# Kernel optimization log

Measured on AMD Instinct MI355X. Metric: run time of the kernel, lower is better.

The kernel has to match this reference:

```python
import jax, jax.numpy as jnp
import numpy as np

HEAD_SIZE = 64

def setup_inputs() -> dict:
    key = jax.random.key(0)
    k1, k2, k3, k4 = jax.random.split(key, 4)
    B, T, C = 4, 4096, 1024
    x = jax.random.normal(k1, (B, T, C), dtype=jnp.float32)
    Wk = jax.random.normal(k2, (C, HEAD_SIZE), dtype=jnp.float32) * (C ** -0.5)
    Wq = jax.random.normal(k3, (C, HEAD_SIZE), dtype=jnp.float32) * (C ** -0.5)
    Wv = jax.random.normal(k4, (C, HEAD_SIZE), dtype=jnp.float32) * (C ** -0.5)
    return {"x": x, "Wk": Wk, "Wq": Wq, "Wv": Wv}

def reference(x, Wk, Wq, Wv):
    # x: [B, T, C]; projections to [B, T, H]
    T = x.shape[1]
    k = jnp.einsum('btc,ch->bth', x, Wk)
    q = jnp.einsum('btc,ch->bth', x, Wq)
    v = jnp.einsum('btc,ch->bth', x, Wv)
    scale = jnp.asarray(HEAD_SIZE ** -0.5, dtype=x.dtype)
    scores = jnp.einsum('bqh,bkh->bqk', q, k) * scale  # [B, T, T]
    causal = jnp.tril(jnp.ones((T, T), dtype=bool))
    scores = jnp.where(causal, scores, jnp.asarray(-jnp.inf, dtype=scores.dtype))
    attn = jax.nn.softmax(scores, axis=-1)  # dropout is identity in eval mode
    out = jnp.einsum('bqk,bkh->bqh', attn, v)
    return out
```

## Files before the change

### kernel.cpp

```cpp
#include <hip/hip_runtime.h>
#include <hip/hip_bf16.h>
#include <math.h>

#define NB 4
#define NT 4096
#define NC 1024
#define NH 64

typedef __attribute__((ext_vector_type(8))) short short8;
typedef __attribute__((ext_vector_type(4))) float f32x4;
typedef __attribute__((ext_vector_type(8))) unsigned short ushort8v;
typedef __attribute__((ext_vector_type(4))) unsigned short ushort4v;

static __device__ __forceinline__ unsigned short f2bf(float f) {
    union { __hip_bfloat16 b; unsigned short u; } cv;
    cv.b = __float2bfloat16(f);
    return cv.u;
}

__global__ __launch_bounds__(256) void wprep_kernel(
    const float* __restrict__ Wk,
    const float* __restrict__ Wq,
    const float* __restrict__ Wv,
    unsigned short* __restrict__ wt)
{
    __shared__ float tile[64][65];
    const int m  = blockIdx.x >> 4;
    const int k0 = (blockIdx.x & 15) << 6;
    const float* __restrict__ W = (m == 0) ? Wk : (m == 1) ? Wq : Wv;
    const float qs = (m == 1) ? 0.125f * 1.44269504f : 1.0f;
    const int tid = threadIdx.x;
    const int c   = tid & 63;
    for (int i = tid >> 6; i < 64; i += 4)
        tile[i][c] = W[(size_t)(k0 + i) * NH + c];
    __syncthreads();
    const int i0 = (tid >> 6) * 16;
    unsigned short* dst = wt + ((size_t)m * 64 + c) * NC + k0 + i0;
    ushort8v a, b;
#pragma unroll
    for (int j = 0; j < 8; ++j) a[j] = f2bf(tile[i0 + j][c] * qs);
#pragma unroll
    for (int j = 0; j < 8; ++j) b[j] = f2bf(tile[i0 + 8 + j][c] * qs);
    *reinterpret_cast<ushort8v*>(dst)     = a;
    *reinterpret_cast<ushort8v*>(dst + 8) = b;
}

__global__ __launch_bounds__(256, 2) void proj_kernel(
    const float* __restrict__ x,
    const unsigned short* __restrict__ wt,
    unsigned short* __restrict__ ko,
    unsigned short* __restrict__ qo,
    unsigned short* __restrict__ vt)
{
    __shared__ unsigned short xsb[2][32 * 64];
    __shared__ unsigned short wsb[2][192 * 64];

    const int tid  = threadIdx.x;
    const int wid  = tid >> 6;
    const int lane = tid & 63;
    const int l15  = lane & 15;
    const int hi   = lane >> 4;
    const int t0   = blockIdx.x << 5;

    const int srow = tid >> 3;
    const int sg   = tid & 7;
    const int ssw  = sg ^ (srow & 7);
    const float* __restrict__ xsrc = x + (size_t)(t0 + srow) * NC + sg * 8;
    unsigned short* const sdst0 = &xsb[0][srow * 64 + ssw * 8];
    unsigned short* const sdst1 = &xsb[1][srow * 64 + ssw * 8];

    int wrow[6], wsl[6];
#pragma unroll
    for (int it = 0; it < 6; ++it) {
        const int F = it * 256 + tid;
        wrow[it] = F >> 3;
        wsl[it]  = F & 7;
    }

    int mm[3], hr[3];
#pragma unroll
    for (int f = 0; f < 3; ++f) {
        const int hc = wid * 48 + f * 16;
        mm[f] = hc >> 6;
        hr[f] = hc & 63;
    }

    f32x4 acc[2][3];
#pragma unroll
    for (int mf = 0; mf < 2; ++mf)
#pragma unroll
        for (int f = 0; f < 3; ++f) acc[mf][f] = (f32x4){0.f, 0.f, 0.f, 0.f};

    auto XWRITE = [&](unsigned short* dst, const f32x4& a, const f32x4& b) {
        ushort8v pk;
        pk[0] = f2bf(a[0]); pk[1] = f2bf(a[1]);
        pk[2] = f2bf(a[2]); pk[3] = f2bf(a[3]);
        pk[4] = f2bf(b[0]); pk[5] = f2bf(b[1]);
        pk[6] = f2bf(b[2]); pk[7] = f2bf(b[3]);
        *reinterpret_cast<ushort8v*>(dst) = pk;
    };

    auto WSTORE = [&](int bi, const short8 (&wr)[6]) {
#pragma unroll
        for (int it = 0; it < 6; ++it) {
            const int dst = wrow[it] * 64 + ((wsl[it] ^ (wrow[it] & 7)) << 3);
            *reinterpret_cast<short8*>(&wsb[bi][dst]) = wr[it];
        }
    };

    auto COMPUTE = [&](int bi) {
        short8 xf[2][2];
#pragma unroll
        for (int mf = 0; mf < 2; ++mf) {
            const int row = mf * 16 + l15;
#pragma unroll
            for (int ks = 0; ks < 2; ++ks) {
                const int sw = (ks * 4 + hi) ^ (row & 7);
                xf[mf][ks] = *reinterpret_cast<const short8*>(
                    &xsb[bi][row * 64 + sw * 8]);
            }
        }
#pragma unroll
        for (int f = 0; f < 3; ++f) {
            const int wr = wid * 48 + f * 16 + l15;
            const int r7 = l15 & 7;
#pragma unroll
            for (int ks = 0; ks < 2; ++ks) {
                const short8 wf = *reinterpret_cast<const short8*>(
                    &wsb[bi][wr * 64 + (((hi + ks * 4) ^ r7) << 3)]);
                if (mm[f] == 2) {
#pragma unroll
                    for (int mf = 0; mf < 2; ++mf)
                        acc[mf][f] = __builtin_amdgcn_mfma_f32_16x16x32_bf16(
                            xf[mf][ks], wf, acc[mf][f], 0, 0, 0);
                } else {
#pragma unroll
                    for (int mf = 0; mf < 2; ++mf)
                        acc[mf][f] = __builtin_amdgcn_mfma_f32_16x16x32_bf16(
                            wf, xf[mf][ks], acc[mf][f], 0, 0, 0);
                }
            }
        }
    };

    {
        const f32x4 a = *reinterpret_cast<const f32x4*>(xsrc);
        const f32x4 b = *reinterpret_cast<const f32x4*>(xsrc + 4);
        XWRITE(sdst0, a, b);
        short8 wr[6];
#pragma unroll
        for (int it = 0; it < 6; ++it)
            wr[it] = *reinterpret_cast<const short8*>(
                wt + (size_t)wrow[it] * NC + wsl[it] * 8);
        WSTORE(0, wr);
    }
    __syncthreads();

    for (int ck = 0; ck < 16; ++ck) {
        const int cur = ck & 1;
        f32x4 na, nb;
        short8 wr[6];
        if (ck < 15) {
            const float* p = xsrc + (ck + 1) * 64;
            na = *reinterpret_cast<const f32x4*>(p);
            nb = *reinterpret_cast<const f32x4*>(p + 4);
#pragma unroll
            for (int it = 0; it < 6; ++it)
                wr[it] = *reinterpret_cast<const short8*>(
                    wt + (size_t)wrow[it] * NC + (ck + 1) * 64 + wsl[it] * 8);
        }
        COMPUTE(cur);
        if (ck < 15) {
            XWRITE(cur ? sdst0 : sdst1, na, nb);
            WSTORE(cur ^ 1, wr);
        }
        __syncthreads();
    }

    const int b  = t0 >> 12;
    const int tl = t0 & (NT - 1);
#pragma unroll
    for (int f = 0; f < 3; ++f) {
#pragma unroll
        for (int mf = 0; mf < 2; ++mf) {
            const f32x4 a = acc[mf][f];
            ushort4v pk;
            pk[0] = f2bf(a[0]); pk[1] = f2bf(a[1]);
            pk[2] = f2bf(a[2]); pk[3] = f2bf(a[3]);
            if (mm[f] == 2) {
                unsigned short* d = vt + ((size_t)(b * NH + hr[f] + l15)) * NT
                                       + tl + mf * 16 + hi * 4;
                *reinterpret_cast<ushort4v*>(d) = pk;
            } else {
                unsigned short* o = (mm[f] == 0) ? ko : qo;
                unsigned short* d = o + (size_t)(t0 + mf * 16 + l15) * NH
                                      + hr[f] + hi * 4;
                *reinterpret_cast<ushort4v*>(d) = pk;
            }
        }
    }
}

__global__ __launch_bounds__(512) void attn_kernel(
    const unsigned short* __restrict__ kin,
    const unsigned short* __restrict__ qin,
    const unsigned short* __restrict__ vt,
    float* __restrict__ part)
{
    __shared__ unsigned short ksb[2][64 * 64];
    __shared__ unsigned short vsb[2][64 * 64];
    __shared__ unsigned short p_lds[8][16 * 72];

    const int tid  = threadIdx.x;
    const int wid  = tid >> 6;
    const int lane = tid & 63;
    const int q15  = lane & 15;
    const int hi   = lane >> 4;

    const int bid  = blockIdx.x;
    const int xcd  = bid & 7;
    const int b    = xcd >> 1;
    const int clin = ((bid >> 3) << 1) | (xcd & 1);
    const int c    = 143 - clin;

    int qi = 0, basei = 0;
    for (int t = 31; t >= 0; --t) {
        const int g = t >> 2, r = t & 3;
        const int bs = t + 2 * g * (g - 1) + r * g;
        if (bs <= c) { qi = t; basei = bs; break; }
    }
    const int k     = c - basei;
    const int n_blk = 2 * qi + 2;
    const int jb0   = k * 8;
    const int jend  = min(jb0 + 8, n_blk);
    const int n_w   = 2 * qi + 1 + (wid >> 2);

    const unsigned short* kb = kin + (size_t)b * NT * NH;
    const unsigned short* qb = qin + (size_t)b * NT * NH;
    const unsigned short* vb = vt  + (size_t)b * NH * NT;

    const int gq = qi * 128 + wid * 16 + q15;

    short8 qf0, qf1;
    {
        const unsigned short* qrow = qb + (size_t)gq * NH + hi * 8;
        qf0 = *reinterpret_cast<const short8*>(qrow);
        qf1 = *reinterpret_cast<const short8*>(qrow + 32);
    }

    const int srow = tid >> 3;
    const int sg   = tid & 7;
    const int sdst = srow * 64 + (sg ^ (srow & 7)) * 8;
    const unsigned short* kstat = kb + (size_t)srow * NH + sg * 8;
    const unsigned short* vstat = vb + (size_t)srow * NT + sg * 8;

    f32x4 ot[4];
#pragma unroll
    for (int i = 0; i < 4; ++i) ot[i] = (f32x4){0.f, 0.f, 0.f, 0.f};
    float m = 0.f, lp = 0.f;

    {
        const short8 kr = *reinterpret_cast<const short8*>(kstat + (size_t)jb0 * 4096);
        const short8 vr = *reinterpret_cast<const short8*>(vstat + jb0 * 64);
        *reinterpret_cast<short8*>(&ksb[0][sdst]) = kr;
        *reinterpret_cast<short8*>(&vsb[0][sdst]) = vr;
    }
    __syncthreads();

    int cur = 0;
    for (int jb = jb0; jb < jend; ++jb) {
        const bool more = (jb + 1 < jend);
        short8 knx, vnx;
        if (more) {
            knx = *reinterpret_cast<const short8*>(kstat + (size_t)(jb + 1) * 4096);
            vnx = *reinterpret_cast<const short8*>(vstat + (jb + 1) * 64);
        }

        if (jb < n_w) {
            const int kv0 = jb << 6;
            const int r7  = q15 & 7;

            f32x4 st[4];
#pragma unroll
            for (int kt = 0; kt < 4; ++kt) {
                const int rb = (kt * 16 + q15) * 64;
                const short8 ka0 = *reinterpret_cast<const short8*>(
                    &ksb[cur][rb + ((hi ^ r7) * 8)]);
                const short8 ka1 = *reinterpret_cast<const short8*>(
                    &ksb[cur][rb + (((4 + hi) ^ r7) * 8)]);
                f32x4 acc = (f32x4){0.f, 0.f, 0.f, 0.f};
                acc = __builtin_amdgcn_mfma_f32_16x16x32_bf16(ka0, qf0, acc, 0, 0, 0);
                acc = __builtin_amdgcn_mfma_f32_16x16x32_bf16(ka1, qf1, acc, 0, 0, 0);
                st[kt] = acc;
            }

            float tmax4 = -INFINITY;
            if (jb == n_w - 1) {
#pragma unroll
                for (int kt = 0; kt < 4; ++kt)
#pragma unroll
                    for (int r = 0; r < 4; ++r) {
                        const int gk = kv0 + kt * 16 + hi * 4 + r;
                        const float s = (gk <= gq) ? st[kt][r] : -INFINITY;
                        st[kt][r] = s;
                        tmax4 = fmaxf(tmax4, s);
                    }
            } else {
#pragma unroll
                for (int kt = 0; kt < 4; ++kt)
#pragma unroll
                    for (int r = 0; r < 4; ++r)
                        tmax4 = fmaxf(tmax4, st[kt][r]);
            }

            if (!__all(tmax4 <= m + 11.5f)) {
                float tm = fmaxf(tmax4, __shfl_xor(tmax4, 16));
                tm = fmaxf(tm, __shfl_xor(tm, 32));
                const float mnew = fmaxf(m, tm);
                const float corr = __builtin_amdgcn_exp2f(m - mnew);
                lp *= corr;
#pragma unroll
                for (int i = 0; i < 4; ++i) {
                    ot[i][0] *= corr; ot[i][1] *= corr;
                    ot[i][2] *= corr; ot[i][3] *= corr;
                }
                m = mnew;
            }

#pragma unroll
            for (int kt = 0; kt < 4; ++kt) {
                const float p0 = __builtin_amdgcn_exp2f(st[kt][0] - m);
                const float p1 = __builtin_amdgcn_exp2f(st[kt][1] - m);
                const float p2 = __builtin_amdgcn_exp2f(st[kt][2] - m);
                const float p3 = __builtin_amdgcn_exp2f(st[kt][3] - m);
                lp += (p0 + p1) + (p2 + p3);
                ushort4v pk;
                pk[0] = f2bf(p0); pk[1] = f2bf(p1);
                pk[2] = f2bf(p2); pk[3] = f2bf(p3);
                *reinterpret_cast<ushort4v*>(&p_lds[wid][q15 * 72 + kt * 16 + hi * 4]) = pk;
            }

            const short8 pb0 = *reinterpret_cast<const short8*>(&p_lds[wid][q15 * 72 + hi * 8]);
            const short8 pb1 = *reinterpret_cast<const short8*>(&p_lds[wid][q15 * 72 + 32 + hi * 8]);
#pragma unroll
            for (int ht = 0; ht < 4; ++ht) {
                const int rb = (ht * 16 + q15) * 64;
                const short8 va0 = *reinterpret_cast<const short8*>(
                    &vsb[cur][rb + ((hi ^ r7) * 8)]);
                const short8 va1 = *reinterpret_cast<const short8*>(
                    &vsb[cur][rb + (((4 + hi) ^ r7) * 8)]);
                ot[ht] = __builtin_amdgcn_mfma_f32_16x16x32_bf16(va0, pb0, ot[ht], 0, 0, 0);
                ot[ht] = __builtin_amdgcn_mfma_f32_16x16x32_bf16(va1, pb1, ot[ht], 0, 0, 0);
            }
        }

        if (more) {
            *reinterpret_cast<short8*>(&ksb[cur ^ 1][sdst]) = knx;
            *reinterpret_cast<short8*>(&vsb[cur ^ 1][sdst]) = vnx;
        }
        __syncthreads();
        cur ^= 1;
    }

    float l = lp + __shfl_xor(lp, 16);
    l += __shfl_xor(l, 32);
    float* pp = part + (((size_t)b * 144 + c) * 128 + wid * 16 + q15) * 68;
#pragma unroll
    for (int ht = 0; ht < 4; ++ht)
        *reinterpret_cast<f32x4*>(pp + ht * 16 + hi * 4) = ot[ht];
    if (hi == 0) { pp[64] = m; pp[65] = l; }
}

__global__ __launch_bounds__(256) void comb_kernel(
    const float* __restrict__ part,
    float* __restrict__ outp)
{
    const int tid = threadIdx.x;
    const int bid = blockIdx.x;
    const int b   = bid >> 10;
    const int lr  = ((bid & 1023) << 2) + (tid >> 6);
    const int h   = tid & 63;
    const int qi  = lr >> 7;
    const int g   = qi >> 2, r = qi & 3;
    const int basei = qi + 2 * g * (g - 1) + r * g;
    const int nch   = (qi >> 2) + 1;
    const float* p0 = part + (((size_t)b * 144 + basei) * 128 + (lr & 127)) * 68;

    float mg = -INFINITY;
    for (int ch = 0; ch < nch; ++ch)
        mg = fmaxf(mg, p0[(size_t)ch * 128 * 68 + 64]);
    float L = 0.f, o = 0.f;
    for (int ch = 0; ch < nch; ++ch) {
        const float* pc = p0 + (size_t)ch * 128 * 68;
        const float w = __builtin_amdgcn_exp2f(pc[64] - mg);
        L += w * pc[65];
        o += w * pc[h];
    }
    outp[((size_t)b * NT + lr) * NH + h] = o / L;
}

extern "C" void kernel_launch(void* const* d_in, const int* in_sizes, int n_in,
                              void* d_out, int out_size, void* d_ws, size_t ws_size,
                              hipStream_t stream) {
    const float* x  = (const float*)d_in[0];
    const float* Wk = (const float*)d_in[1];
    const float* Wq = (const float*)d_in[2];
    const float* Wv = (const float*)d_in[3];
    float* out = (float*)d_out;

    unsigned short* kbuf = (unsigned short*)d_ws;
    unsigned short* qbuf = kbuf + (size_t)NB * NT * NH;
    unsigned short* vtbf = qbuf + (size_t)NB * NT * NH;
    unsigned short* wtbf = vtbf + (size_t)NB * NT * NH;
    float* part = (float*)(wtbf + (size_t)3 * 64 * NC);

    wprep_kernel<<<48, 256, 0, stream>>>(Wk, Wq, Wv, wtbf);
    proj_kernel<<<NB * NT / 32, 256, 0, stream>>>(x, wtbf, kbuf, qbuf, vtbf);
    attn_kernel<<<576, 512, 0, stream>>>(kbuf, qbuf, vtbf, part);
    comb_kernel<<<4096, 256, 0, stream>>>(part, out);
}
```

Before: 67.10 us.

## Process two query tiles per wave in attention, halving block size

Each wave now handles 32 query rows as two 16-row tiles instead of one, so a block of 4 waves (256 threads) covers the same 128 queries that 8 waves did before. Every K/V fragment read from LDS is reused for two MFMA groups, halving LDS traffic per FLOP, and each thread stages two rows of K/V per tile. The cost is more registers per thread (two accumulators, score sets and softmax states) and fewer waves per block to hide latency.

Measured after the change: 73.02 us. 8.8% more time.

```diff
diff --git a/kernel.cpp b/kernel.cpp
--- a/kernel.cpp
+++ b/kernel.cpp
@@ -6,6 +6,7 @@
 #define NT 4096
 #define NC 1024
 #define NH 64
+#define NCH 144
 
 typedef __attribute__((ext_vector_type(8))) short short8;
 typedef __attribute__((ext_vector_type(4))) float f32x4;
@@ -201,7 +202,7 @@
     }
 }
 
-__global__ __launch_bounds__(512) void attn_kernel(
+__global__ __launch_bounds__(256) void attn_kernel(
     const unsigned short* __restrict__ kin,
     const unsigned short* __restrict__ qin,
     const unsigned short* __restrict__ vt,
@@ -221,7 +222,7 @@
     const int xcd  = bid & 7;
     const int b    = xcd >> 1;
     const int clin = ((bid >> 3) << 1) | (xcd & 1);
-    const int c    = 143 - clin;
+    const int c    = (NCH - 1) - clin;
 
     int qi = 0, basei = 0;
     for (int t = 31; t >= 0; --t) {
@@ -233,54 +234,67 @@
     const int n_blk = 2 * qi + 2;
     const int jb0   = k * 8;
     const int jend  = min(jb0 + 8, n_blk);
-    const int n_w   = 2 * qi + 1 + (wid >> 2);
+    const int n_w   = 2 * qi + 1 + (wid >> 1);
 
     const unsigned short* kb = kin + (size_t)b * NT * NH;
     const unsigned short* qb = qin + (size_t)b * NT * NH;
     const unsigned short* vb = vt  + (size_t)b * NH * NT;
 
-    const int gq = qi * 128 + wid * 16 + q15;
-
-    short8 qf0, qf1;
-    {
-        const unsigned short* qrow = qb + (size_t)gq * NH + hi * 8;
-        qf0 = *reinterpret_cast<const short8*>(qrow);
-        qf1 = *reinterpret_cast<const short8*>(qrow + 32);
+    const int gqb = qi * 128 + wid * 32 + q15;
+
+    short8 qf[2][2];
+#pragma unroll
+    for (int qc = 0; qc < 2; ++qc) {
+        const unsigned short* qrow = qb + (size_t)(gqb + qc * 16) * NH + hi * 8;
+        qf[qc][0] = *reinterpret_cast<const short8*>(qrow);
+        qf[qc][1] = *reinterpret_cast<const short8*>(qrow + 32);
     }
 
     const int srow = tid >> 3;
     const int sg   = tid & 7;
-    const int sdst = srow * 64 + (sg ^ (srow & 7)) * 8;
-    const unsigned short* kstat = kb + (size_t)srow * NH + sg * 8;
-    const unsigned short* vstat = vb + (size_t)srow * NT + sg * 8;
-
-    f32x4 ot[4];
-#pragma unroll
-    for (int i = 0; i < 4; ++i) ot[i] = (f32x4){0.f, 0.f, 0.f, 0.f};
-    float m = 0.f, lp = 0.f;
+    const int ssw  = (sg ^ (srow & 7)) * 8;
+    const int sdA  = srow * 64 + ssw;
+    const int sdB  = (srow + 32) * 64 + ssw;
+    const unsigned short* kstA = kb + (size_t)srow * NH + sg * 8;
+    const unsigned short* kstB = kb + (size_t)(srow + 32) * NH + sg * 8;
+    const unsigned short* vstA = vb + (size_t)srow * NT + sg * 8;
+    const unsigned short* vstB = vb + (size_t)(srow + 32) * NT + sg * 8;
+
+    f32x4 ot[2][4];
+#pragma unroll
+    for (int qc = 0; qc < 2; ++qc)
+#pragma unroll
+        for (int i = 0; i < 4; ++i) ot[qc][i] = (f32x4){0.f, 0.f, 0.f, 0.f};
+    float m0 = 0.f, m1 = 0.f, lp0 = 0.f, lp1 = 0.f;
 
     {
-        const short8 kr = *reinterpret_cast<const short8*>(kstat + (size_t)jb0 * 4096);
-        const short8 vr = *reinterpret_cast<const short8*>(vstat + jb0 * 64);
-        *reinterpret_cast<short8*>(&ksb[0][sdst]) = kr;
-        *reinterpret_cast<short8*>(&vsb[0][sdst]) = vr;
+        *reinterpret_cast<short8*>(&ksb[0][sdA]) =
+            *reinterpret_cast<const short8*>(kstA + (size_t)jb0 * 4096);
+        *reinterpret_cast<short8*>(&ksb[0][sdB]) =
+            *reinterpret_cast<const short8*>(kstB + (size_t)jb0 * 4096);
+        *reinterpret_cast<short8*>(&vsb[0][sdA]) =
+            *reinterpret_cast<const short8*>(vstA + jb0 * 64);
+        *reinterpret_cast<short8*>(&vsb[0][sdB]) =
+            *reinterpret_cast<const short8*>(vstB + jb0 * 64);
     }
     __syncthreads();
 
     int cur = 0;
     for (int jb = jb0; jb < jend; ++jb) {
         const bool more = (jb + 1 < jend);
-        short8 knx, vnx;
+        short8 ka_n, kb_n, va_n, vb_n;
         if (more) {
-            knx = *reinterpret_cast<const short8*>(kstat + (size_t)(jb + 1) * 4096);
-            vnx = *reinterpret_cast<const short8*>(vstat + (jb + 1) * 64);
+            ka_n = *reinterpret_cast<const short8*>(kstA + (size_t)(jb + 1) * 4096);
+            kb_n = *reinterpret_cast<const short8*>(kstB + (size_t)(jb + 1) * 4096);
+            va_n = *reinterpret_cast<const short8*>(vstA + (jb + 1) * 64);
+            vb_n = *reinterpret_cast<const short8*>(vstB + (jb + 1) * 64);
         }
 
         if (jb < n_w) {
             const int kv0 = jb << 6;
             const int r7  = q15 & 7;
 
-            f32x4 st[4];
+            f32x4 st[2][4];
 #pragma unroll
             for (int kt = 0; kt < 4; ++kt) {
                 const int rb = (kt * 16 + q15) * 64;
@@ -288,60 +302,88 @@
                     &ksb[cur][rb + ((hi ^ r7) * 8)]);
                 const short8 ka1 = *reinterpret_cast<const short8*>(
                     &ksb[cur][rb + (((4 + hi) ^ r7) * 8)]);
-                f32x4 acc = (f32x4){0.f, 0.f, 0.f, 0.f};
-                acc = __builtin_amdgcn_mfma_f32_16x16x32_bf16(ka0, qf0, acc, 0, 0, 0);
-                acc = __builtin_amdgcn_mfma_f32_16x16x32_bf16(ka1, qf1, acc, 0, 0, 0);
-                st[kt] = acc;
-            }
-
-            float tmax4 = -INFINITY;
+#pragma unroll
+                for (int qc = 0; qc < 2; ++qc) {
+                    f32x4 acc = (f32x4){0.f, 0.f, 0.f, 0.f};
+                    acc = __builtin_amdgcn_mfma_f32_16x16x32_bf16(ka0, qf[qc][0], acc, 0, 0, 0);
+                    acc = __builtin_amdgcn_mfma_f32_16x16x32_bf16(ka1, qf[qc][1], acc, 0, 0, 0);
+                    st[qc][kt] = acc;
+                }
+            }
+
+            float tx0 = -INFINITY, tx1 = -INFINITY;
             if (jb == n_w - 1) {
 #pragma unroll
                 for (int kt = 0; kt < 4; ++kt)
 #pragma unroll
                     for (int r = 0; r < 4; ++r) {
                         const int gk = kv0 + kt * 16 + hi * 4 + r;
-                        const float s = (gk <= gq) ? st[kt][r] : -INFINITY;
-                        st[kt][r] = s;
-                        tmax4 = fmaxf(tmax4, s);
+                        float s0 = (gk <= gqb)      ? st[0][kt][r] : -INFINITY;
+                        float s1 = (gk <= gqb + 16) ? st[1][kt][r] : -INFINITY;
+                        st[0][kt][r] = s0; st[1][kt][r] = s1;
+                        tx0 = fmaxf(tx0, s0); tx1 = fmaxf(tx1, s1);
                     }
             } else {
 #pragma unroll
                 for (int kt = 0; kt < 4; ++kt)
 #pragma unroll
-                    for (int r = 0; r < 4; ++r)
-                        tmax4 = fmaxf(tmax4, st[kt][r]);
-            }
-
-            if (!__all(tmax4 <= m + 11.5f)) {
-                float tm = fmaxf(tmax4, __shfl_xor(tmax4, 16));
+                    for (int r = 0; r < 4; ++r) {
+                        tx0 = fmaxf(tx0, st[0][kt][r]);
+                        tx1 = fmaxf(tx1, st[1][kt][r]);
+                    }
+            }
+
+            if (!__all(tx0 <= m0 + 11.5f)) {
+                float tm = fmaxf(tx0, __shfl_xor(tx0, 16));
                 tm = fmaxf(tm, __shfl_xor(tm, 32));
-                const float mnew = fmaxf(m, tm);
-                const float corr = __builtin_amdgcn_exp2f(m - mnew);
-                lp *= corr;
+                const float mnew = fmaxf(m0, tm);
+                const float corr = __builtin_amdgcn_exp2f(m0 - mnew);
+                lp0 *= corr;
 #pragma unroll
                 for (int i = 0; i < 4; ++i) {
-                    ot[i][0] *= corr; ot[i][1] *= corr;
-                    ot[i][2] *= corr; ot[i][3] *= corr;
+                    ot[0][i][0] *= corr; ot[0][i][1] *= corr;
+                    ot[0][i][2] *= corr; ot[0][i][3] *= corr;
                 }
-                m = mnew;
-            }
-
-#pragma unroll
-            for (int kt = 0; kt < 4; ++kt) {
-                const float p0 = __builtin_amdgcn_exp2f(st[kt][0] - m);
-                const float p1 = __builtin_amdgcn_exp2f(st[kt][1] - m);
-                const float p2 = __builtin_amdgcn_exp2f(st[kt][2] - m);
-                const float p3 = __builtin_amdgcn_exp2f(st[kt][3] - m);
-                lp += (p0 + p1) + (p2 + p3);
-                ushort4v pk;
-                pk[0] = f2bf(p0); pk[1] = f2bf(p1);
-                pk[2] = f2bf(p2); pk[3] = f2bf(p3);
-                *reinterpret_cast<ushort4v*>(&p_lds[wid][q15 * 72 + kt * 16 + hi * 4]) = pk;
-            }
-
-            const short8 pb0 = *reinterpret_cast<const short8*>(&p_lds[wid][q15 * 72 + hi * 8]);
-            const short8 pb1 = *reinterpret_cast<const short8*>(&p_lds[wid][q15 * 72 + 32 + hi * 8]);
+                m0 = mnew;
+            }
+            if (!__all(tx1 <= m1 + 11.5f)) {
+                float tm = fmaxf(tx1, __shfl_xor(tx1, 16));
+                tm = fmaxf(tm, __shfl_xor(tm, 32));
+                const float mnew = fmaxf(m1, tm);
+                const float corr = __builtin_amdgcn_exp2f(m1 - mnew);
+                lp1 *= corr;
+#pragma unroll
+                for (int i = 0; i < 4; ++i) {
+                    ot[1][i][0] *= corr; ot[1][i][1] *= corr;
+                    ot[1][i][2] *= corr; ot[1][i][3] *= corr;
+                }
+                m1 = mnew;
+            }
+
+#pragma unroll
+            for (int qc = 0; qc < 2; ++qc) {
+                const float mq = qc ? m1 : m0;
+                float lps = 0.f;
+                unsigned short* pr = &p_lds[wid * 2 + qc][0];
+#pragma unroll
+                for (int kt = 0; kt < 4; ++kt) {
+                    const float p0 = __builtin_amdgcn_exp2f(st[qc][kt][0] - mq);
+                    const float p1 = __builtin_amdgcn_exp2f(st[qc][kt][1] - mq);
+                    const float p2 = __builtin_amdgcn_exp2f(st[qc][kt][2] - mq);
+                    const float p3 = __builtin_amdgcn_exp2f(st[qc][kt][3] - mq);
+                    lps += (p0 + p1) + (p2 + p3);
+                    ushort4v pk;
+                    pk[0] = f2bf(p0); pk[1] = f2bf(p1);
+                    pk[2] = f2bf(p2); pk[3] = f2bf(p3);
+                    *reinterpret_cast<ushort4v*>(pr + q15 * 72 + kt * 16 + hi * 4) = pk;
+                }
+                if (qc) lp1 += lps; else lp0 += lps;
+            }
+
+            const short8 pb00 = *reinterpret_cast<const short8*>(&p_lds[wid * 2][q15 * 72 + hi * 8]);
+            const short8 pb01 = *reinterpret_cast<const short8*>(&p_lds[wid * 2][q15 * 72 + 32 + hi * 8]);
+            const short8 pb10 = *reinterpret_cast<const short8*>(&p_lds[wid * 2 + 1][q15 * 72 + hi * 8]);
+            const short8 pb11 = *reinterpret_cast<const short8*>(&p_lds[wid * 2 + 1][q15 * 72 + 32 + hi * 8]);
 #pragma unroll
             for (int ht = 0; ht < 4; ++ht) {
                 const int rb = (ht * 16 + q15) * 64;
@@ -349,26 +391,38 @@
                     &vsb[cur][rb + ((hi ^ r7) * 8)]);
                 const short8 va1 = *reinterpret_cast<const short8*>(
                     &vsb[cur][rb + (((4 + hi) ^ r7) * 8)]);
-                ot[ht] = __builtin_amdgcn_mfma_f32_16x16x32_bf16(va0, pb0, ot[ht], 0, 0, 0);
-                ot[ht] = __builtin_amdgcn_mfma_f32_16x16x32_bf16(va1, pb1, ot[ht], 0, 0, 0);
+                ot[0][ht] = __builtin_amdgcn_mfma_f32_16x16x32_bf16(va0, pb00, ot[0][ht], 0, 0, 0);
+                ot[0][ht] = __builtin_amdgcn_mfma_f32_16x16x32_bf16(va1, pb01, ot[0][ht], 0, 0, 0);
+                ot[1][ht] = __builtin_amdgcn_mfma_f32_16x16x32_bf16(va0, pb10, ot[1][ht], 0, 0, 0);
+                ot[1][ht] = __builtin_amdgcn_mfma_f32_16x16x32_bf16(va1, pb11, ot[1][ht], 0, 0, 0);
             }
         }
 
         if (more) {
-            *reinterpret_cast<short8*>(&ksb[cur ^ 1][sdst]) = knx;
-            *reinterpret_cast<short8*>(&vsb[cur ^ 1][sdst]) = vnx;
+            *reinterpret_cast<short8*>(&ksb[cur ^ 1][sdA]) = ka_n;
+            *reinterpret_cast<short8*>(&ksb[cur ^ 1][sdB]) = kb_n;
+            *reinterpret_cast<short8*>(&vsb[cur ^ 1][sdA]) = va_n;
+            *reinterpret_cast<short8*>(&vsb[cur ^ 1][sdB]) = vb_n;
         }
         __syncthreads();
         cur ^= 1;
     }
 
-    float l = lp + __shfl_xor(lp, 16);
-    l += __shfl_xor(l, 32);
-    float* pp = part + (((size_t)b * 144 + c) * 128 + wid * 16 + q15) * 68;
-#pragma unroll
-    for (int ht = 0; ht < 4; ++ht)
-        *reinterpret_cast<f32x4*>(pp + ht * 16 + hi * 4) = ot[ht];
-    if (hi == 0) { pp[64] = m; pp[65] = l; }
+    float l0 = lp0 + __shfl_xor(lp0, 16);
+    l0 += __shfl_xor(l0, 32);
+    float l1 = lp1 + __shfl_xor(lp1, 16);
+    l1 += __shfl_xor(l1, 32);
+#pragma unroll
+    for (int qc = 0; qc < 2; ++qc) {
+        float* pp = part + (((size_t)b * NCH + c) * 128 + wid * 32 + qc * 16 + q15) * 68;
+#pragma unroll
+        for (int ht = 0; ht < 4; ++ht)
+            *reinterpret_cast<f32x4*>(pp + ht * 16 + hi * 4) = ot[qc][ht];
+        if (hi == 0) {
+            pp[64] = qc ? m1 : m0;
+            pp[65] = qc ? l1 : l0;
+        }
+    }
 }
 
 __global__ __launch_bounds__(256) void comb_kernel(
@@ -384,7 +438,7 @@
     const int g   = qi >> 2, r = qi & 3;
     const int basei = qi + 2 * g * (g - 1) + r * g;
     const int nch   = (qi >> 2) + 1;
-    const float* p0 = part + (((size_t)b * 144 + basei) * 128 + (lr & 127)) * 68;
+    const float* p0 = part + (((size_t)b * NCH + basei) * 128 + (lr & 127)) * 68;
 
     float mg = -INFINITY;
     for (int ch = 0; ch < nch; ++ch)
@@ -416,6 +470,6 @@
 
     wprep_kernel<<<48, 256, 0, stream>>>(Wk, Wq, Wv, wtbf);
     proj_kernel<<<NB * NT / 32, 256, 0, stream>>>(x, wtbf, kbuf, qbuf, vtbf);
-    attn_kernel<<<576, 512, 0, stream>>>(kbuf, qbuf, vtbf, part);
+    attn_kernel<<<576, 256, 0, stream>>>(kbuf, qbuf, vtbf, part);
     comb_kernel<<<4096, 256, 0, stream>>>(part, out);
 }
```
